# Performance work log

Hardware: AMD Instinct MI355X
Metric: run time of the kernel (lower is better)

## Reference

```python
import jax, jax.numpy as jnp
import numpy as np

BATCH, IN_DIM, HID, OUT_DIM, Z = 8192, 2048, 4096, 2048, 4
CONN_P = 0.5  # Bernoulli keep-probability y


def random_activation(h, ids):
    # ids: [dim] int32 in [0,5); per-channel nonlinearity applied over batch.
    ids = ids[None, :]
    return jnp.select(
        [ids == 0, ids == 1, ids == 2, ids == 3],
        [jax.nn.relu(h), jax.nn.sigmoid(h), jnp.tanh(h), jnp.where(h >= 0, h, 0.1 * h)],
        jax.nn.selu(h),
    )


def _make_linear(key, fan_in, fan_out):
    kw, kb, km = jax.random.split(key, 3)
    w = jax.random.normal(kw, (fan_out, fan_in), dtype=jnp.float32)
    mask = jax.random.bernoulli(km, CONN_P, (fan_out, fan_in)).astype(jnp.float32)
    b = jax.random.normal(kb, (fan_out,), dtype=jnp.float32)
    return w * mask, b


def setup_inputs() -> dict:
    key = jax.random.key(0)
    ks = jax.random.split(key, 16)
    inp = {"input_pattern": jax.random.normal(ks[0], (BATCH, IN_DIM), dtype=jnp.float32)}
    dims = [(IN_DIM, HID)] + [(HID, HID)] * Z + [(HID, OUT_DIM)]  # z+2 Linear layers
    for i, (fi, fo) in enumerate(dims):
        w, b = _make_linear(ks[1 + i], fi, fo)
        inp[f"w{i}"] = w
        inp[f"b{i}"] = b
        inp[f"ids{i}"] = jax.random.randint(ks[8 + i], (fo,), 0, 5, dtype=jnp.int32)
    return inp


def reference(input_pattern, w0, b0, ids0, w1, b1, ids1, w2, b2, ids2,
              w3, b3, ids3, w4, b4, ids4, w5, b5, ids5):
    ws = (w0, w1, w2, w3, w4, w5)
    bs = (b0, b1, b2, b3, b4, b5)
    ids = (ids0, ids1, ids2, ids3, ids4, ids5)
    h = input_pattern
    for w, b, i in zip(ws, bs, ids):
        h = random_activation(h @ w.T + b, i)
    return h
```

## Files before the change

### kernel.cpp

```cpp
#include <hip/hip_runtime.h>

typedef _Float16 f16;
typedef _Float16 f16x8 __attribute__((ext_vector_type(8)));
typedef float f32x4 __attribute__((ext_vector_type(4)));

__device__ __forceinline__ void gload_lds16(const void* g, void* l) {
  __builtin_amdgcn_global_load_lds(
      (const __attribute__((address_space(1))) void*)g,
      (__attribute__((address_space(3))) void*)l, 16, 0, 0);
}

__device__ __forceinline__ float act_apply(float x, int id) {
  switch (id) {
    case 0: return fmaxf(x, 0.0f);
    case 1: return 1.0f / (1.0f + __expf(-x));
    case 2: return tanhf(x);
    case 3: return x >= 0.0f ? x : 0.1f * x;
    default: return 1.0507009873554805f *
                    (x > 0.0f ? x : 1.6732632423543772f * expm1f(x));
  }
}

template <bool FINAL>
__global__ __launch_bounds__(512, 2)
void gemm_bias_act(const f16* __restrict__ A, const f16* __restrict__ W,
                   const float* __restrict__ bias, const int* __restrict__ ids,
                   float Sa, float invSn, void* __restrict__ outv,
                   int M, int N, int K) {
  __shared__ f16 lA[4][256 * 32];
  __shared__ f16 lB[4][256 * 32];

  const int tid  = (int)threadIdx.x;
  const int lane = tid & 63;
  const int wid  = tid >> 6;
  const int wm   = wid >> 2;
  const int wn   = wid & 3;

  const int nbx = N >> 8;
  const int nwg = (M >> 8) * nbx;
  const int b   = (int)blockIdx.x;
  const int swz = (b & 7) * (nwg >> 3) + (b >> 3);
  const int brow = (swz / nbx) << 8;
  const int bcol = (swz % nbx) << 8;

  const int d0 = tid << 4;
  const int d1 = d0 + 8192;
  const int s0 = d0 ^ (((d0 >> 7) & 7) << 4);
  const int s1 = d1 ^ (((d1 >> 7) & 7) << 4);
  const int r0 = s0 >> 6, c0 = (s0 >> 4) & 3;
  const int r1 = s1 >> 6, c1 = (s1 >> 4) & 3;

  const f16* pA0 = A + (long)(brow + r0) * K + c0 * 8;
  const f16* pA1 = A + (long)(brow + r1) * K + c1 * 8;
  const f16* pB0 = W + (long)(bcol + r0) * K + c0 * 8;
  const f16* pB1 = W + (long)(bcol + r1) * K + c1 * 8;
  const int e0 = tid << 3;
  const int e1 = e0 + 4096;

  const int fr = lane & 15;
  const int kb = lane >> 4;
  const int xorv = ((fr >> 1) & 7) << 4;
  const char* baA = (const char*)&lA[0][0];
  const char* baB = (const char*)&lB[0][0];

  int offA[8], offB[4];
#pragma unroll
  for (int m = 0; m < 8; ++m)
    offA[m] = (((wm * 128 + m * 16 + fr) << 6) + (kb << 4)) ^ xorv;
#pragma unroll
  for (int n = 0; n < 4; ++n)
    offB[n] = (((wn * 64 + n * 16 + fr) << 6) + (kb << 4)) ^ xorv;

  f32x4 acc[8][4];
#pragma unroll
  for (int m = 0; m < 8; ++m)
#pragma unroll
    for (int n = 0; n < 4; ++n) acc[m][n] = (f32x4){0.f, 0.f, 0.f, 0.f};

  const int nt = K >> 5;

#pragma unroll
  for (int t = 0; t < 3; ++t) {
    const long kk = (long)t << 5;
    gload_lds16(pA0 + kk, &lA[t][e0]);
    gload_lds16(pA1 + kk, &lA[t][e1]);
    gload_lds16(pB0 + kk, &lB[t][e0]);
    gload_lds16(pB1 + kk, &lB[t][e1]);
  }
  asm volatile("s_waitcnt vmcnt(8)" ::: "memory");
  __builtin_amdgcn_s_barrier();
  asm volatile("" ::: "memory");

  f16x8 afA[4], afB[4], bf[4];
#pragma unroll
  for (int m = 0; m < 4; ++m) afA[m] = *(const f16x8*)(baA + offA[m]);
#pragma unroll
  for (int n = 0; n < 4; ++n) bf[n]  = *(const f16x8*)(baB + offB[n]);

  for (int i = 0; i < nt; ++i) {
    const int so  = (i & 3) << 14;
    const int so2 = ((i + 1) & 3) << 14;
    const int ps  = (i + 3) & 3;
    const long kk3 = (long)(i + 3) << 5;
    const bool pf = (i + 3) < nt;

#pragma unroll
    for (int m = 0; m < 4; ++m)
      afB[m] = *(const f16x8*)(baA + so + offA[m + 4]);
    if (pf) {
      gload_lds16(pA0 + kk3, &lA[ps][e0]);
      gload_lds16(pB0 + kk3, &lB[ps][e0]);
    }
    __builtin_amdgcn_s_setprio(1);
#pragma unroll
    for (int m = 0; m < 4; ++m)
#pragma unroll
      for (int n = 0; n < 4; ++n)
        acc[m][n] = __builtin_amdgcn_mfma_f32_16x16x32_f16(afA[m], bf[n],
                                                           acc[m][n], 0, 0, 0);
    __builtin_amdgcn_s_setprio(0);
    asm volatile("" ::: "memory");
    __builtin_amdgcn_s_barrier();
    asm volatile("" ::: "memory");

    if (i < nt - 1) {
      if (i < nt - 3)       asm volatile("s_waitcnt vmcnt(6)" ::: "memory");
      else if (i == nt - 3) asm volatile("s_waitcnt vmcnt(4)" ::: "memory");
      else                  asm volatile("s_waitcnt vmcnt(0)" ::: "memory");
      __builtin_amdgcn_s_barrier();
      asm volatile("" ::: "memory");
    }
    __builtin_amdgcn_s_setprio(1);
#pragma unroll
    for (int m = 0; m < 4; ++m)
#pragma unroll
      for (int n = 0; n < 4; ++n)
        acc[4 + m][n] = __builtin_amdgcn_mfma_f32_16x16x32_f16(afB[m], bf[n],
                                                               acc[4 + m][n],
                                                               0, 0, 0);
    __builtin_amdgcn_s_setprio(0);
    if (i < nt - 1) {
#pragma unroll
      for (int m = 0; m < 4; ++m)
        afA[m] = *(const f16x8*)(baA + so2 + offA[m]);
#pragma unroll
      for (int n = 0; n < 4; ++n)
        bf[n] = *(const f16x8*)(baB + so2 + offB[n]);
      if (pf) {
        gload_lds16(pA1 + kk3, &lA[ps][e1]);
        gload_lds16(pB1 + kk3, &lB[ps][e1]);
      }
      asm volatile("" ::: "memory");
      __builtin_amdgcn_s_barrier();
      asm volatile("" ::: "memory");
    }
  }

  const int r4 = (lane >> 4) << 2;
#pragma unroll
  for (int n = 0; n < 4; ++n) {
    const int gcol = bcol + wn * 64 + n * 16 + fr;
    const float bv = bias[gcol];
    const int id   = ids[gcol];
#pragma unroll
    for (int m = 0; m < 8; ++m) {
      const int grow = brow + wm * 128 + m * 16 + r4;
#pragma unroll
      for (int i = 0; i < 4; ++i) {
        const float y = act_apply(acc[m][n][i] * Sa + bv, id);
        if (FINAL) {
          ((float*)outv)[(long)(grow + i) * N + gcol] = y;
        } else {
          ((f16*)outv)[(long)(grow + i) * N + gcol] = (f16)(y * invSn);
        }
      }
    }
  }
}

__global__ void cvt_f32_to_f16(const float* __restrict__ in, f16* __restrict__ out,
                               float scale, int n) {
  int i = ((int)blockIdx.x * 256 + (int)threadIdx.x) * 8;
  const int stride = (int)gridDim.x * 256 * 8;
  for (; i < n; i += stride) {
    const float4 v0 = *(const float4*)(in + i);
    const float4 v1 = *(const float4*)(in + i + 4);
    f16x8 h;
    h[0] = (f16)(v0.x * scale); h[1] = (f16)(v0.y * scale);
    h[2] = (f16)(v0.z * scale); h[3] = (f16)(v0.w * scale);
    h[4] = (f16)(v1.x * scale); h[5] = (f16)(v1.y * scale);
    h[6] = (f16)(v1.z * scale); h[7] = (f16)(v1.w * scale);
    *(f16x8*)(out + i) = h;
  }
}

extern "C" void kernel_launch(void* const* d_in, const int* in_sizes, int n_in,
                              void* d_out, int out_size, void* d_ws, size_t ws_size,
                              hipStream_t stream) {
  (void)in_sizes; (void)n_in; (void)out_size; (void)ws_size;
  const int M = 8192, IND = 2048, HID = 4096, OUTD = 2048;
  const float* x = (const float*)d_in[0];

  f16* actA = (f16*)d_ws;
  f16* actB = actA + (size_t)M * HID;
  f16* wbuf = actB + (size_t)M * HID;

  const float S[6] = {1.f, 16.f, 512.f, 16384.f, 262144.f, 8388608.f};

  const int Ks[6] = {IND, HID, HID, HID, HID, HID};
  const int Ns[6] = {HID, HID, HID, HID, HID, OUTD};

  cvt_f32_to_f16<<<2048, 256, 0, stream>>>(x, actA, 1.0f, M * IND);

  f16* cur = actA;
  f16* nxt = actB;
  for (int i = 0; i < 6; ++i) {
    const int K = Ks[i], N = Ns[i];
    const float* w  = (const float*)d_in[1 + 3 * i];
    const float* bs = (const float*)d_in[2 + 3 * i];
    const int* id   = (const int*)d_in[3 + 3 * i];

    cvt_f32_to_f16<<<2048, 256, 0, stream>>>(w, wbuf, 1.0f, N * K);

    const int nblk = (M >> 8) * (N >> 8);
    if (i < 5) {
      gemm_bias_act<false><<<nblk, 512, 0, stream>>>(
          cur, wbuf, bs, id, S[i], 1.0f / S[i + 1], nxt, M, N, K);
      f16* t = cur; cur = nxt; nxt = t;
    } else {
      gemm_bias_act<true><<<nblk, 512, 0, stream>>>(
          cur, wbuf, bs, id, S[i], 1.0f, d_out, M, N, K);
    }
  }
}
```

Before: 1.951 ms.

## Switch GEMM to 32x32x16 MFMA tiles with two-phase K pipeline

```diff
diff --git a/kernel.cpp b/kernel.cpp
--- a/kernel.cpp
+++ b/kernel.cpp
@@ -2,7 +2,7 @@
 
 typedef _Float16 f16;
 typedef _Float16 f16x8 __attribute__((ext_vector_type(8)));
-typedef float f32x4 __attribute__((ext_vector_type(4)));
+typedef float f32x16 __attribute__((ext_vector_type(16)));
 
 __device__ __forceinline__ void gload_lds16(const void* g, void* l) {
   __builtin_amdgcn_global_load_lds(
@@ -57,25 +57,31 @@
   const int e0 = tid << 3;
   const int e1 = e0 + 4096;
 
-  const int fr = lane & 15;
-  const int kb = lane >> 4;
-  const int xorv = ((fr >> 1) & 7) << 4;
+  const int l31 = lane & 31;
+  const int lhi = lane >> 5;
+  const int xorv = ((l31 >> 1) & 7) << 4;
   const char* baA = (const char*)&lA[0][0];
   const char* baB = (const char*)&lB[0][0];
 
-  int offA[8], offB[4];
-#pragma unroll
-  for (int m = 0; m < 8; ++m)
-    offA[m] = (((wm * 128 + m * 16 + fr) << 6) + (kb << 4)) ^ xorv;
-#pragma unroll
-  for (int n = 0; n < 4; ++n)
-    offB[n] = (((wn * 64 + n * 16 + fr) << 6) + (kb << 4)) ^ xorv;
-
-  f32x4 acc[8][4];
-#pragma unroll
-  for (int m = 0; m < 8; ++m)
-#pragma unroll
-    for (int n = 0; n < 4; ++n) acc[m][n] = (f32x4){0.f, 0.f, 0.f, 0.f};
+  int offA[4][2], offB[2][2];
+#pragma unroll
+  for (int m = 0; m < 4; ++m)
+#pragma unroll
+    for (int kh = 0; kh < 2; ++kh)
+      offA[m][kh] = (((wm * 128 + m * 32 + l31) << 6) + ((2 * kh + lhi) << 4)) ^ xorv;
+#pragma unroll
+  for (int n = 0; n < 2; ++n)
+#pragma unroll
+    for (int kh = 0; kh < 2; ++kh)
+      offB[n][kh] = (((wn * 64 + n * 32 + l31) << 6) + ((2 * kh + lhi) << 4)) ^ xorv;
+
+  f32x16 acc[4][2];
+#pragma unroll
+  for (int m = 0; m < 4; ++m)
+#pragma unroll
+    for (int n = 0; n < 2; ++n)
+#pragma unroll
+      for (int r = 0; r < 16; ++r) acc[m][n][r] = 0.0f;
 
   const int nt = K >> 5;
 
@@ -91,87 +97,82 @@
   __builtin_amdgcn_s_barrier();
   asm volatile("" ::: "memory");
 
-  f16x8 afA[4], afB[4], bf[4];
-#pragma unroll
-  for (int m = 0; m < 4; ++m) afA[m] = *(const f16x8*)(baA + offA[m]);
-#pragma unroll
-  for (int n = 0; n < 4; ++n) bf[n]  = *(const f16x8*)(baB + offB[n]);
-
   for (int i = 0; i < nt; ++i) {
     const int so  = (i & 3) << 14;
-    const int so2 = ((i + 1) & 3) << 14;
     const int ps  = (i + 3) & 3;
     const long kk3 = (long)(i + 3) << 5;
     const bool pf = (i + 3) < nt;
 
-#pragma unroll
-    for (int m = 0; m < 4; ++m)
-      afB[m] = *(const f16x8*)(baA + so + offA[m + 4]);
+    f16x8 af[4], bf[2];
+
+#pragma unroll
+    for (int m = 0; m < 4; ++m) af[m] = *(const f16x8*)(baA + so + offA[m][0]);
+#pragma unroll
+    for (int n = 0; n < 2; ++n) bf[n] = *(const f16x8*)(baB + so + offB[n][0]);
     if (pf) {
       gload_lds16(pA0 + kk3, &lA[ps][e0]);
       gload_lds16(pB0 + kk3, &lB[ps][e0]);
     }
+    __builtin_amdgcn_s_barrier();
+    asm volatile("s_waitcnt lgkmcnt(0)" ::: "memory");
+    __builtin_amdgcn_sched_barrier(0);
     __builtin_amdgcn_s_setprio(1);
 #pragma unroll
     for (int m = 0; m < 4; ++m)
 #pragma unroll
-      for (int n = 0; n < 4; ++n)
-        acc[m][n] = __builtin_amdgcn_mfma_f32_16x16x32_f16(afA[m], bf[n],
+      for (int n = 0; n < 2; ++n)
+        acc[m][n] = __builtin_amdgcn_mfma_f32_32x32x16_f16(af[m], bf[n],
                                                            acc[m][n], 0, 0, 0);
     __builtin_amdgcn_s_setprio(0);
-    asm volatile("" ::: "memory");
+    __builtin_amdgcn_sched_barrier(0);
     __builtin_amdgcn_s_barrier();
-    asm volatile("" ::: "memory");
+
+#pragma unroll
+    for (int m = 0; m < 4; ++m) af[m] = *(const f16x8*)(baA + so + offA[m][1]);
+#pragma unroll
+    for (int n = 0; n < 2; ++n) bf[n] = *(const f16x8*)(baB + so + offB[n][1]);
+    if (pf) {
+      gload_lds16(pA1 + kk3, &lA[ps][e1]);
+      gload_lds16(pB1 + kk3, &lB[ps][e1]);
+    }
+    __builtin_amdgcn_s_barrier();
+    asm volatile("s_waitcnt lgkmcnt(0)" ::: "memory");
+    __builtin_amdgcn_sched_barrier(0);
+    __builtin_amdgcn_s_setprio(1);
+#pragma unroll
+    for (int m = 0; m < 4; ++m)
+#pragma unroll
+      for (int n = 0; n < 2; ++n)
+        acc[m][n] = __builtin_amdgcn_mfma_f32_32x32x16_f16(af[m], bf[n],
+                                                           acc[m][n], 0, 0, 0);
+    __builtin_amdgcn_s_setprio(0);
+    __builtin_amdgcn_sched_barrier(0);
 
     if (i < nt - 1) {
-      if (i < nt - 3)       asm volatile("s_waitcnt vmcnt(6)" ::: "memory");
+      if (i <= nt - 4)      asm volatile("s_waitcnt vmcnt(8)" ::: "memory");
       else if (i == nt - 3) asm volatile("s_waitcnt vmcnt(4)" ::: "memory");
       else                  asm volatile("s_waitcnt vmcnt(0)" ::: "memory");
       __builtin_amdgcn_s_barrier();
       asm volatile("" ::: "memory");
     }
-    __builtin_amdgcn_s_setprio(1);
-#pragma unroll
-    for (int m = 0; m < 4; ++m)
-#pragma unroll
-      for (int n = 0; n < 4; ++n)
-        acc[4 + m][n] = __builtin_amdgcn_mfma_f32_16x16x32_f16(afB[m], bf[n],
-                                                               acc[4 + m][n],
-                                                               0, 0, 0);
-    __builtin_amdgcn_s_setprio(0);
-    if (i < nt - 1) {
-#pragma unroll
-      for (int m = 0; m < 4; ++m)
-        afA[m] = *(const f16x8*)(baA + so2 + offA[m]);
-#pragma unroll
-      for (int n = 0; n < 4; ++n)
-        bf[n] = *(const f16x8*)(baB + so2 + offB[n]);
-      if (pf) {
-        gload_lds16(pA1 + kk3, &lA[ps][e1]);
-        gload_lds16(pB1 + kk3, &lB[ps][e1]);
-      }
-      asm volatile("" ::: "memory");
-      __builtin_amdgcn_s_barrier();
-      asm volatile("" ::: "memory");
-    }
-  }
-
-  const int r4 = (lane >> 4) << 2;
-#pragma unroll
-  for (int n = 0; n < 4; ++n) {
-    const int gcol = bcol + wn * 64 + n * 16 + fr;
+  }
+
+#pragma unroll
+  for (int n = 0; n < 2; ++n) {
+    const int gcol = bcol + wn * 64 + n * 32 + l31;
     const float bv = bias[gcol];
     const int id   = ids[gcol];
 #pragma unroll
-    for (int m = 0; m < 8; ++m) {
-      const int grow = brow + wm * 128 + m * 16 + r4;
-#pragma unroll
-      for (int i = 0; i < 4; ++i) {
-        const float y = act_apply(acc[m][n][i] * Sa + bv, id);
+    for (int m = 0; m < 4; ++m) {
+      const int rbase = brow + wm * 128 + m * 32 + 4 * lhi;
+#pragma unroll
+      for (int r = 0; r < 16; ++r) {
+        const int grow = rbase + (r & 3) + 8 * (r >> 2);
+        const float y = act_apply(acc[m][n][r] * Sa + bv, id);
         if (FINAL) {
-          ((float*)outv)[(long)(grow + i) * N + gcol] = y;
+          ((float*)outv)[(long)grow * N + gcol] = y;
         } else {
-          ((f16*)outv)[(long)(grow + i) * N + gcol] = (f16)(y * invSn);
+          ((f16*)outv)[(long)grow * N + gcol] = (f16)(y * invSn);
         }
       }
     }
```

Result: slower. 2.072 ms (+6.2%).

## Restructure GEMM main loop into two barrier-separated half-stages with split A/B prefetch

Applied to the files above, without the earlier changes.

```diff
diff --git a/kernel.cpp b/kernel.cpp
--- a/kernel.cpp
+++ b/kernel.cpp
@@ -91,70 +91,55 @@
   __builtin_amdgcn_s_barrier();
   asm volatile("" ::: "memory");
 
-  f16x8 afA[4], afB[4], bf[4];
-#pragma unroll
-  for (int m = 0; m < 4; ++m) afA[m] = *(const f16x8*)(baA + offA[m]);
-#pragma unroll
-  for (int n = 0; n < 4; ++n) bf[n]  = *(const f16x8*)(baB + offB[n]);
-
-  for (int i = 0; i < nt; ++i) {
-    const int so  = (i & 3) << 14;
-    const int so2 = ((i + 1) & 3) << 14;
-    const int ps  = (i + 3) & 3;
-    const long kk3 = (long)(i + 3) << 5;
-    const bool pf = (i + 3) < nt;
-
+  for (int s = 0; s < nt; ++s) {
+    const int so  = (s & 3) << 14;
+    const int ps  = (s + 3 < nt) ? (s + 3) : (nt - 1);
+    const int pso = ps & 3;
+    const long kk = (long)ps << 5;
+
+    f16x8 af[4], bf[4];
+
+#pragma unroll
+    for (int m = 0; m < 4; ++m) af[m] = *(const f16x8*)(baA + so + offA[m]);
+#pragma unroll
+    for (int n = 0; n < 4; ++n) bf[n] = *(const f16x8*)(baB + so + offB[n]);
+    gload_lds16(pA0 + kk, &lA[pso][e0]);
+    gload_lds16(pA1 + kk, &lA[pso][e1]);
+    if (!(s & 1)) asm volatile("s_waitcnt vmcnt(6)" ::: "memory");
+    __builtin_amdgcn_s_barrier();
+    asm volatile("s_waitcnt lgkmcnt(0)" ::: "memory");
+    __builtin_amdgcn_sched_barrier(0);
+    __builtin_amdgcn_s_setprio(1);
 #pragma unroll
     for (int m = 0; m < 4; ++m)
-      afB[m] = *(const f16x8*)(baA + so + offA[m + 4]);
-    if (pf) {
-      gload_lds16(pA0 + kk3, &lA[ps][e0]);
-      gload_lds16(pB0 + kk3, &lB[ps][e0]);
-    }
-    __builtin_amdgcn_s_setprio(1);
-#pragma unroll
-    for (int m = 0; m < 4; ++m)
 #pragma unroll
       for (int n = 0; n < 4; ++n)
-        acc[m][n] = __builtin_amdgcn_mfma_f32_16x16x32_f16(afA[m], bf[n],
+        acc[m][n] = __builtin_amdgcn_mfma_f32_16x16x32_f16(af[m], bf[n],
                                                            acc[m][n], 0, 0, 0);
     __builtin_amdgcn_s_setprio(0);
-    asm volatile("" ::: "memory");
-    __builtin_amdgcn_s_barrier();
-    asm volatile("" ::: "memory");
-
-    if (i < nt - 1) {
-      if (i < nt - 3)       asm volatile("s_waitcnt vmcnt(6)" ::: "memory");
-      else if (i == nt - 3) asm volatile("s_waitcnt vmcnt(4)" ::: "memory");
-      else                  asm volatile("s_waitcnt vmcnt(0)" ::: "memory");
-      __builtin_amdgcn_s_barrier();
-      asm volatile("" ::: "memory");
-    }
+    __builtin_amdgcn_sched_barrier(0);
+    __builtin_amdgcn_s_barrier();
+
+#pragma unroll
+    for (int m = 0; m < 4; ++m) af[m] = *(const f16x8*)(baA + so + offA[m + 4]);
+    gload_lds16(pB0 + kk, &lB[pso][e0]);
+    gload_lds16(pB1 + kk, &lB[pso][e1]);
+    __builtin_amdgcn_s_barrier();
+    asm volatile("s_waitcnt lgkmcnt(0)" ::: "memory");
+    __builtin_amdgcn_sched_barrier(0);
     __builtin_amdgcn_s_setprio(1);
 #pragma unroll
     for (int m = 0; m < 4; ++m)
 #pragma unroll
       for (int n = 0; n < 4; ++n)
-        acc[4 + m][n] = __builtin_amdgcn_mfma_f32_16x16x32_f16(afB[m], bf[n],
+        acc[4 + m][n] = __builtin_amdgcn_mfma_f32_16x16x32_f16(af[m], bf[n],
                                                                acc[4 + m][n],
                                                                0, 0, 0);
     __builtin_amdgcn_s_setprio(0);
-    if (i < nt - 1) {
-#pragma unroll
-      for (int m = 0; m < 4; ++m)
-        afA[m] = *(const f16x8*)(baA + so2 + offA[m]);
-#pragma unroll
-      for (int n = 0; n < 4; ++n)
-        bf[n] = *(const f16x8*)(baB + so2 + offB[n]);
-      if (pf) {
-        gload_lds16(pA1 + kk3, &lA[ps][e1]);
-        gload_lds16(pB1 + kk3, &lB[ps][e1]);
-      }
-      asm volatile("" ::: "memory");
-      __builtin_amdgcn_s_barrier();
-      asm volatile("" ::: "memory");
-    }
-  }
+    __builtin_amdgcn_sched_barrier(0);
+    __builtin_amdgcn_s_barrier();
+  }
+  asm volatile("s_waitcnt vmcnt(0)" ::: "memory");
 
   const int r4 = (lane >> 4) << 2;
 #pragma unroll
```

New measurement: 2.139 ms. 9.6% more time.
